# Kernel optimization log

Hardware: AMD Instinct MI355X
Metric: run time of the kernel (lower is better)

The kernel has to match this reference:

```python
import jax, jax.numpy as jnp
import numpy as np

H = 1024  # hidden_size == input_size

def lstm_cell(x_t, h, c, W_ih, W_hh, b):
    # gates: [B, 4H] in torch order (input, forget, cell, output)
    gates = x_t @ W_ih.T + h @ W_hh.T + b
    i, f, g, o = jnp.split(gates, 4, axis=-1)
    c_new = jax.nn.sigmoid(f) * c + jax.nn.sigmoid(i) * jnp.tanh(g)
    h_new = jax.nn.sigmoid(o) * jnp.tanh(c_new)
    return h_new, c_new

def setup_inputs() -> dict:
    key = jax.random.key(0)
    ks = jax.random.split(key, 7)
    S, B = 512, 64
    std = 1.0 / np.sqrt(H)  # torch LSTMCell init scale
    return {
        "x": jax.random.normal(ks[0], (S, B, H), jnp.float32),
        "hx0": jax.random.normal(ks[1], (B, H), jnp.float32),
        "cx0": jax.random.normal(ks[2], (B, H), jnp.float32),
        "W_ih": jax.random.uniform(ks[3], (4 * H, H), jnp.float32, -std, std),
        "W_hh": jax.random.uniform(ks[4], (4 * H, H), jnp.float32, -std, std),
        "b_ih": jax.random.uniform(ks[5], (4 * H,), jnp.float32, -std, std),
        "b_hh": jax.random.uniform(ks[6], (4 * H,), jnp.float32, -std, std),
    }

def reference(x, hx0, cx0, W_ih, W_hh, b_ih, b_hh):
    b = b_ih + b_hh

    def step(carry, x_t):
        h, c = carry
        h, c = lstm_cell(x_t, h, c, W_ih, W_hh, b)
        return (h, c), None

    (h, c), _ = jax.lax.scan(step, (hx0, cx0), x)
    outputs = []
    for _ in range(2):
        h, c = lstm_cell(h, h, c, W_ih, W_hh, b)
        outputs.append(h)
    return jnp.stack(outputs)  # [2, B, H]
```

## Files before the change

kernel.cpp:

```cpp
#include <hip/hip_runtime.h>

#define SEQ 512
#define TOT 514
#define BH  65536
#define NBUF (TOT + 1)

typedef _Float16 f16x8 __attribute__((ext_vector_type(8)));
typedef float f32x4 __attribute__((ext_vector_type(4)));

__device__ __forceinline__ unsigned short f2h_bits(float f) {
  union { _Float16 h; unsigned short s; } u; u.h = (_Float16)f; return u.s;
}

__device__ __forceinline__ float fast_sigmoid(float x) {
  return 1.f / (1.f + __expf(-x));
}
__device__ __forceinline__ float fast_tanh(float x) {
  float e = __expf(-2.f * fabsf(x));
  float r = (1.f - e) / (1.f + e);
  return copysignf(r, x);
}

__device__ __forceinline__ unsigned long long dirty16(unsigned long long u) {
  unsigned long long n = ~u;
  return (n - 0x0001000100010001ULL) & ~n & 0x8000800080008000ULL;
}

__global__ void cvt_kernel(const float* __restrict__ x, const float* __restrict__ hx0,
                           unsigned short* __restrict__ X16, unsigned short* __restrict__ H0) {
  const long long n4x = (long long)SEQ * BH / 4;
  const long long n4h = BH / 4;
  const long long stride = (long long)gridDim.x * blockDim.x;
  for (long long i = (long long)blockIdx.x * blockDim.x + threadIdx.x;
       i < n4x + n4h; i += stride) {
    const float* src; unsigned short* dst;
    if (i < n4x) {
      src = x + 4 * i; dst = X16 + 4 * i;
    } else {
      long long e = (i - n4x) * 4;
      int u0 = e & 15, r = (e >> 4) & 15, sl = (e >> 8) & 63, qq = (int)(e >> 14);
      src = hx0 + (qq * 16 + r) * 1024 + sl * 16 + u0;
      dst = H0 + e;
    }
    float4 v = *(const float4*)src;
    union { unsigned short s[4]; unsigned long long u; } pk;
    pk.s[0] = f2h_bits(v.x); pk.s[1] = f2h_bits(v.y);
    pk.s[2] = f2h_bits(v.z); pk.s[3] = f2h_bits(v.w);
    *(unsigned long long*)dst = pk.u;
  }
}

__global__ __launch_bounds__(256, 1)
void lstm_kernel(const float* __restrict__ cx0,
                 const float* __restrict__ W_ih, const float* __restrict__ W_hh,
                 const float* __restrict__ b_ih, const float* __restrict__ b_hh,
                 const unsigned short* __restrict__ X16,
                 unsigned short* __restrict__ H16,
                 float* __restrict__ out) {
  __shared__ float red[2][4][16][68];

  const int tid  = threadIdx.x;
  const int wave = tid >> 6;
  const int lane = tid & 63;
  const int u16v = lane & 15;
  const int q4   = lane >> 4;
  const int q    = blockIdx.x >> 6;
  const int s    = blockIdx.x & 63;
  const int ub   = s * 16;
  const int kb   = wave * 256;

  f16x8 bfx[4][8], bfh[4][8];
#pragma unroll
  for (int g = 0; g < 4; ++g) {
    const float* wi = W_ih + (size_t)((g << 10) + ub + u16v) * 1024 + kb + q4 * 8;
    const float* wh = W_hh + (size_t)((g << 10) + ub + u16v) * 1024 + kb + q4 * 8;
#pragma unroll
    for (int i = 0; i < 8; ++i) {
      float4 x0 = *(const float4*)(wi + i * 32);
      float4 x1 = *(const float4*)(wi + i * 32 + 4);
      float4 h0 = *(const float4*)(wh + i * 32);
      float4 h1 = *(const float4*)(wh + i * 32 + 4);
      f16x8 bx, bh;
      bx[0] = (_Float16)x0.x; bx[1] = (_Float16)x0.y; bx[2] = (_Float16)x0.z; bx[3] = (_Float16)x0.w;
      bx[4] = (_Float16)x1.x; bx[5] = (_Float16)x1.y; bx[6] = (_Float16)x1.z; bx[7] = (_Float16)x1.w;
      bh[0] = (_Float16)h0.x; bh[1] = (_Float16)h0.y; bh[2] = (_Float16)h0.z; bh[3] = (_Float16)h0.w;
      bh[4] = (_Float16)h1.x; bh[5] = (_Float16)h1.y; bh[6] = (_Float16)h1.z; bh[7] = (_Float16)h1.w;
      bfx[g][i] = bx; bfh[g][i] = bh;
    }
  }

  const int er = tid >> 4, eu = tid & 15;
  const int rge = q * 16 + er;
  float c = cx0[rge * 1024 + ub + eu];
  const float bi  = b_ih[       ub + eu] + b_hh[       ub + eu];
  const float bfg = b_ih[1024 + ub + eu] + b_hh[1024 + ub + eu];
  const float bg  = b_ih[2048 + ub + eu] + b_hh[2048 + ub + eu];
  const float bo  = b_ih[3072 + ub + eu] + b_hh[3072 + ub + eu];

  const size_t xbase = (size_t)(q * 16 + u16v) * 1024 + kb + q4 * 8;
  const size_t hfrag = ((size_t)(q * 64 + wave * 16 + (q4 >> 1)) << 8)
                       + u16v * 16 + (q4 & 1) * 8;
  const size_t puboff = ((size_t)(q * 64 + s) << 8) + tid;

  for (int t = 0; t < TOT; ++t) {
    f32x4 a0 = {0.f, 0.f, 0.f, 0.f}, a1 = a0, a2 = a0, a3 = a0;

    if (t < SEQ) {
      const unsigned short* xs = X16 + (size_t)t * BH + xbase;
      f16x8 xf[8];
#pragma unroll
      for (int i = 0; i < 8; ++i) xf[i] = *(const f16x8*)(xs + i * 32);
#pragma unroll
      for (int i = 0; i < 8; ++i) {
        a0 = __builtin_amdgcn_mfma_f32_16x16x32_f16(xf[i], bfx[0][i], a0, 0, 0, 0);
        a1 = __builtin_amdgcn_mfma_f32_16x16x32_f16(xf[i], bfx[1][i], a1, 0, 0, 0);
        a2 = __builtin_amdgcn_mfma_f32_16x16x32_f16(xf[i], bfx[2][i], a2, 0, 0, 0);
        a3 = __builtin_amdgcn_mfma_f32_16x16x32_f16(xf[i], bfx[3][i], a3, 0, 0, 0);
      }
    }

    const unsigned short* hs = H16 + (size_t)t * BH + hfrag;
    union { unsigned long long u[2]; f16x8 v; } cv[8];
    while (true) {
#pragma unroll
      for (int i = 0; i < 8; ++i) {
        const unsigned short* p = hs + i * 512;
        cv[i].u[0] = __hip_atomic_load((const unsigned long long*)p,
                                       __ATOMIC_RELAXED, __HIP_MEMORY_SCOPE_AGENT);
        cv[i].u[1] = __hip_atomic_load((const unsigned long long*)(p + 4),
                                       __ATOMIC_RELAXED, __HIP_MEMORY_SCOPE_AGENT);
      }
      unsigned long long agg = 0;
#pragma unroll
      for (int i = 0; i < 8; ++i)
        agg |= dirty16(cv[i].u[0]) | dirty16(cv[i].u[1]);
      if (__all(agg == 0)) break;
    }

    f16x8 hf[8];
#pragma unroll
    for (int i = 0; i < 8; ++i) hf[i] = cv[i].v;
#pragma unroll
    for (int i = 0; i < 8; ++i) {
      a0 = __builtin_amdgcn_mfma_f32_16x16x32_f16(hf[i], bfh[0][i], a0, 0, 0, 0);
      a1 = __builtin_amdgcn_mfma_f32_16x16x32_f16(hf[i], bfh[1][i], a1, 0, 0, 0);
      a2 = __builtin_amdgcn_mfma_f32_16x16x32_f16(hf[i], bfh[2][i], a2, 0, 0, 0);
      a3 = __builtin_amdgcn_mfma_f32_16x16x32_f16(hf[i], bfh[3][i], a3, 0, 0, 0);
    }
    if (t >= SEQ) {
#pragma unroll
      for (int i = 0; i < 8; ++i) {
        a0 = __builtin_amdgcn_mfma_f32_16x16x32_f16(hf[i], bfx[0][i], a0, 0, 0, 0);
        a1 = __builtin_amdgcn_mfma_f32_16x16x32_f16(hf[i], bfx[1][i], a1, 0, 0, 0);
        a2 = __builtin_amdgcn_mfma_f32_16x16x32_f16(hf[i], bfx[2][i], a2, 0, 0, 0);
        a3 = __builtin_amdgcn_mfma_f32_16x16x32_f16(hf[i], bfx[3][i], a3, 0, 0, 0);
      }
    }

    const int par = t & 1;
#pragma unroll
    for (int r = 0; r < 4; ++r) {
      red[par][wave][q4 * 4 + r][     u16v] = a0[r];
      red[par][wave][q4 * 4 + r][16 + u16v] = a1[r];
      red[par][wave][q4 * 4 + r][32 + u16v] = a2[r];
      red[par][wave][q4 * 4 + r][48 + u16v] = a3[r];
    }
    __syncthreads();

    float gi = bi, gf = bfg, gg = bg, go = bo;
#pragma unroll
    for (int w2 = 0; w2 < 4; ++w2) {
      gi += red[par][w2][er][     eu];
      gf += red[par][w2][er][16 + eu];
      gg += red[par][w2][er][32 + eu];
      go += red[par][w2][er][48 + eu];
    }
    c = fast_sigmoid(gf) * c + fast_sigmoid(gi) * fast_tanh(gg);
    float h = fast_sigmoid(go) * fast_tanh(c);

    __hip_atomic_store(H16 + (size_t)(t + 1) * BH + puboff, f2h_bits(h),
                       __ATOMIC_RELAXED, __HIP_MEMORY_SCOPE_AGENT);
    if (t >= SEQ) out[(size_t)(t - SEQ) * BH + rge * 1024 + ub + eu] = h;
  }
}

extern "C" void kernel_launch(void* const* d_in, const int* in_sizes, int n_in,
                              void* d_out, int out_size, void* d_ws, size_t ws_size,
                              hipStream_t stream) {
  const float* x    = (const float*)d_in[0];
  const float* hx0  = (const float*)d_in[1];
  const float* cx0  = (const float*)d_in[2];
  const float* W_ih = (const float*)d_in[3];
  const float* W_hh = (const float*)d_in[4];
  const float* b_ih = (const float*)d_in[5];
  const float* b_hh = (const float*)d_in[6];

  unsigned short* X16 = (unsigned short*)d_ws;
  unsigned short* H16 = X16 + (size_t)SEQ * BH;

  hipMemsetAsync(H16, 0xFF, (size_t)NBUF * BH * sizeof(unsigned short), stream);
  cvt_kernel<<<1024, 256, 0, stream>>>(x, hx0, X16, H16);
  lstm_kernel<<<256, 256, 0, stream>>>(cx0, W_ih, W_hh, b_ih, b_hh,
                                       X16, H16, (float*)d_out);
}
```

Before: 1.994 ms.

## Overlap per-chunk hidden-state polling with MFMA and pack h stores into 64-bit

The spin-wait on the published hidden state now runs one fragment chunk at a time, so the MFMAs for each ready chunk can start while later chunks are still being polled. Before, the whole wave waited until every chunk was clean. Each group of four lanes now combines its fp16 h values with two xor-shuffles and one lane issues a single 64-bit atomic store, instead of four 16-bit stores. This cuts store traffic and shortens the latency of the recurrence's critical path. In exchange it adds per-lane divergent spin loops and shuffle work, and correctness relies on 8-byte atomicity lining up with the consumers' 8-byte reads.

```diff
diff --git a/kernel.cpp b/kernel.cpp
--- a/kernel.cpp
+++ b/kernel.cpp
@@ -121,39 +121,33 @@
 
     const unsigned short* hs = H16 + (size_t)t * BH + hfrag;
     union { unsigned long long u[2]; f16x8 v; } cv[8];
-    while (true) {
-#pragma unroll
-      for (int i = 0; i < 8; ++i) {
+#pragma unroll
+    for (int i = 0; i < 8; ++i) {
+      const unsigned short* p = hs + i * 512;
+      cv[i].u[0] = __hip_atomic_load((const unsigned long long*)p,
+                                     __ATOMIC_RELAXED, __HIP_MEMORY_SCOPE_AGENT);
+      cv[i].u[1] = __hip_atomic_load((const unsigned long long*)(p + 4),
+                                     __ATOMIC_RELAXED, __HIP_MEMORY_SCOPE_AGENT);
+    }
+#pragma unroll
+    for (int i = 0; i < 8; ++i) {
+      while (dirty16(cv[i].u[0]) | dirty16(cv[i].u[1])) {
         const unsigned short* p = hs + i * 512;
         cv[i].u[0] = __hip_atomic_load((const unsigned long long*)p,
                                        __ATOMIC_RELAXED, __HIP_MEMORY_SCOPE_AGENT);
         cv[i].u[1] = __hip_atomic_load((const unsigned long long*)(p + 4),
                                        __ATOMIC_RELAXED, __HIP_MEMORY_SCOPE_AGENT);
       }
-      unsigned long long agg = 0;
-#pragma unroll
-      for (int i = 0; i < 8; ++i)
-        agg |= dirty16(cv[i].u[0]) | dirty16(cv[i].u[1]);
-      if (__all(agg == 0)) break;
-    }
-
-    f16x8 hf[8];
-#pragma unroll
-    for (int i = 0; i < 8; ++i) hf[i] = cv[i].v;
-#pragma unroll
-    for (int i = 0; i < 8; ++i) {
-      a0 = __builtin_amdgcn_mfma_f32_16x16x32_f16(hf[i], bfh[0][i], a0, 0, 0, 0);
-      a1 = __builtin_amdgcn_mfma_f32_16x16x32_f16(hf[i], bfh[1][i], a1, 0, 0, 0);
-      a2 = __builtin_amdgcn_mfma_f32_16x16x32_f16(hf[i], bfh[2][i], a2, 0, 0, 0);
-      a3 = __builtin_amdgcn_mfma_f32_16x16x32_f16(hf[i], bfh[3][i], a3, 0, 0, 0);
-    }
-    if (t >= SEQ) {
-#pragma unroll
-      for (int i = 0; i < 8; ++i) {
-        a0 = __builtin_amdgcn_mfma_f32_16x16x32_f16(hf[i], bfx[0][i], a0, 0, 0, 0);
-        a1 = __builtin_amdgcn_mfma_f32_16x16x32_f16(hf[i], bfx[1][i], a1, 0, 0, 0);
-        a2 = __builtin_amdgcn_mfma_f32_16x16x32_f16(hf[i], bfx[2][i], a2, 0, 0, 0);
-        a3 = __builtin_amdgcn_mfma_f32_16x16x32_f16(hf[i], bfx[3][i], a3, 0, 0, 0);
+      f16x8 hfi = cv[i].v;
+      a0 = __builtin_amdgcn_mfma_f32_16x16x32_f16(hfi, bfh[0][i], a0, 0, 0, 0);
+      a1 = __builtin_amdgcn_mfma_f32_16x16x32_f16(hfi, bfh[1][i], a1, 0, 0, 0);
+      a2 = __builtin_amdgcn_mfma_f32_16x16x32_f16(hfi, bfh[2][i], a2, 0, 0, 0);
+      a3 = __builtin_amdgcn_mfma_f32_16x16x32_f16(hfi, bfh[3][i], a3, 0, 0, 0);
+      if (t >= SEQ) {
+        a0 = __builtin_amdgcn_mfma_f32_16x16x32_f16(hfi, bfx[0][i], a0, 0, 0, 0);
+        a1 = __builtin_amdgcn_mfma_f32_16x16x32_f16(hfi, bfx[1][i], a1, 0, 0, 0);
+        a2 = __builtin_amdgcn_mfma_f32_16x16x32_f16(hfi, bfx[2][i], a2, 0, 0, 0);
+        a3 = __builtin_amdgcn_mfma_f32_16x16x32_f16(hfi, bfx[3][i], a3, 0, 0, 0);
       }
     }
 
@@ -178,8 +172,13 @@
     c = fast_sigmoid(gf) * c + fast_sigmoid(gi) * fast_tanh(gg);
     float h = fast_sigmoid(go) * fast_tanh(c);
 
-    __hip_atomic_store(H16 + (size_t)(t + 1) * BH + puboff, f2h_bits(h),
-                       __ATOMIC_RELAXED, __HIP_MEMORY_SCOPE_AGENT);
+    unsigned hv = f2h_bits(h);
+    unsigned pair = hv | ((unsigned)__shfl_xor((int)hv, 1) << 16);
+    unsigned long long pk = (unsigned long long)pair
+                          | ((unsigned long long)(unsigned)__shfl_xor((int)pair, 2) << 32);
+    if ((eu & 3) == 0)
+      __hip_atomic_store((unsigned long long*)(H16 + (size_t)(t + 1) * BH + puboff),
+                         pk, __ATOMIC_RELAXED, __HIP_MEMORY_SCOPE_AGENT);
     if (t >= SEQ) out[(size_t)(t - SEQ) * BH + rge * 1024 + ub + eu] = h;
   }
 }
```

Result: slower. 2.351 ms (+17.9%).
